# Kernel tuning notes

Measured on AMD Instinct MI355X. Metric: run time of the kernel, lower is better.

## Reference

```python
import jax, jax.numpy as jnp
import numpy as np

N_NODES = 10000
N_EDGES = 640000
D_IN = 128
D_OUT = 128


def setup_inputs() -> dict:
    key = jax.random.key(0)
    k1, k2, k3, k4 = jax.random.split(key, 4)
    x = jax.random.normal(k1, (N_NODES, D_IN), dtype=jnp.float32)
    # PyG GCNConv weight: [dim_out, dim_in] (glorot)
    W = jax.random.normal(k2, (D_OUT, D_IN), dtype=jnp.float32) * (1.0 / np.sqrt(D_IN))
    b = jnp.zeros((D_OUT,), dtype=jnp.float32)
    edge_weight = jax.random.uniform(k3, (N_EDGES,), dtype=jnp.float32)
    edge_index = jax.random.randint(k4, (2, N_EDGES), 0, N_NODES, dtype=jnp.int32)
    return {"x": x, "W": W, "b": b, "edge_weight": edge_weight, "edge_index": edge_index}


def reference(x, W, b, edge_weight, edge_index):
    N = x.shape[0]
    # --- add self loops (fill weight = 1.0), PyG default ---
    loops = jnp.arange(N, dtype=edge_index.dtype)
    src = jnp.concatenate([edge_index[0], loops])
    dst = jnp.concatenate([edge_index[1], loops])
    ew = jnp.concatenate([edge_weight, jnp.ones((N,), dtype=edge_weight.dtype)])
    # --- symmetric GCN normalization: deg from target index ---
    deg = jax.ops.segment_sum(ew, dst, num_segments=N)
    dinv = jnp.where(deg > 0, jax.lax.rsqrt(deg), 0.0)
    norm = dinv[src] * ew * dinv[dst]  # [E+N]
    # --- linear transform then gather-scale-scatter aggregation ---
    h = x @ W.T  # [N, D_OUT]
    msgs = h[src] * norm[:, None]  # [E+N, D_OUT]
    out = jax.ops.segment_sum(msgs, dst, num_segments=N)
    return out + b
```

## Files before the change

### kernel.cpp

```cpp
#include <hip/hip_runtime.h>

#define N_NODES 10000
#define N_EDGES 640000
#define D 128
#define CAP 128

typedef unsigned long long ull;
typedef unsigned short u16;
typedef unsigned int u32;

#define CHUNKS 256
#define EPC 2500
#define GEMM_NPB 32
#define GEMM_BLOCKS ((N_NODES + GEMM_NPB - 1) / GEMM_NPB)
#define SMEM_BYTES 40000
#define EW_FX 131072.0f
#define CNT_SH 24
#define EW_MASK 0xffffffu
#define EWQ_FX 262144.0f
#define SRC_MASK 0x3fffu

__device__ __forceinline__ u16 f2bf(float f) {
    unsigned u = __float_as_uint(f);
    unsigned r = (u + 0x7fffu + ((u >> 16) & 1u)) >> 16;
    return (u16)r;
}


__global__ void __launch_bounds__(256) k_hist_fill_gemm(
    const int* __restrict__ src, const int* __restrict__ dst,
    const float* __restrict__ ew, u32* __restrict__ gcw,
    const float* __restrict__ x, const float* __restrict__ W,
    u16* __restrict__ h_bf, u32* __restrict__ csr)
{
    extern __shared__ char smem[];
    const int t = threadIdx.x;

    if (blockIdx.x < CHUNKS) {
        u32* hist = (u32*)smem;
        for (int i = t; i < N_NODES; i += 256) hist[i] = 0;
        __syncthreads();

        const int e0 = blockIdx.x * EPC;
        u32 dlr[10];
        #pragma unroll
        for (int i = 0; i < 10; ++i) {
            int idx = i * 256 + t;
            dlr[i] = 0xffffffffu;
            if (idx < EPC) {
                int e = e0 + idx;
                int d = dst[e];
                u32 add = (1u << CNT_SH) | (u32)(ew[e] * EW_FX + 0.5f);
                u32 old = atomicAdd(&hist[d], add);
                dlr[i] = ((u32)d << 7) | ((old >> CNT_SH) & 127u);
            }
        }
        __syncthreads();

        for (int i = t; i < N_NODES; i += 256) {
            u32 v = hist[i];
            if (v) {
                u32 old = atomicAdd(&gcw[i], v);
                hist[i] = old >> CNT_SH;
            }
        }
        __syncthreads();

        #pragma unroll
        for (int i = 0; i < 10; ++i) {
            if (dlr[i] != 0xffffffffu) {
                int e = e0 + i * 256 + t;
                int d = (int)(dlr[i] >> 7);
                int lr = (int)(dlr[i] & 127u);
                int slot = (int)hist[d] + lr;
                u32 ewq = (u32)(ew[e] * EWQ_FX);
                csr[(size_t)d * CAP + slot] = (ewq << 14) | (u32)src[e];
            }
        }
    } else {
        float* xs = (float*)smem;
        const int gb = blockIdx.x - CHUNKS;
        const int node0 = gb * GEMM_NPB;
        const int col = t & 127;
        const int half = t >> 7;

        #pragma unroll
        for (int r = 0; r < 16; ++r) {
            int row = half * 16 + r;
            int n = node0 + row;
            xs[row * D + col] = (n < N_NODES) ? x[n * D + col] : 0.0f;
        }
        __syncthreads();

        float acc[16];
        #pragma unroll
        for (int r = 0; r < 16; ++r) acc[r] = 0.0f;

        const float4* Wrow = (const float4*)&W[col * D];
        const float* xbase = &xs[half * 16 * D];
        for (int k4 = 0; k4 < D / 4; ++k4) {
            float4 w = Wrow[k4];
            int k = k4 * 4;
            #pragma unroll
            for (int r = 0; r < 16; ++r) {
                acc[r] += xbase[r * D + k + 0] * w.x;
                acc[r] += xbase[r * D + k + 1] * w.y;
                acc[r] += xbase[r * D + k + 2] * w.z;
                acc[r] += xbase[r * D + k + 3] * w.w;
            }
        }
        #pragma unroll
        for (int r = 0; r < 16; ++r) {
            int n = node0 + half * 16 + r;
            if (n < N_NODES) h_bf[n * D + col] = f2bf(acc[r]);
        }
    }
}


__global__ void __launch_bounds__(256) k_agg(
    const u32* __restrict__ gcw, const u32* __restrict__ csr,
    const u16* __restrict__ h_bf, const float* __restrict__ bias,
    float* __restrict__ out)
{
    const int n = blockIdx.x * 4 + (threadIdx.x >> 6);
    const int lane = threadIdx.x & 63;
    const int slice = lane >> 4;
    const int li = lane & 15;

    const u32 gn = gcw[n];
    const int deg = (int)(gn >> CNT_SH);
    const float dn = rsqrtf(1.0f + (float)(gn & EW_MASK) * (1.0f / EW_FX));
    const u32* bucket = csr + (size_t)n * CAP;

    float acc[8];
    #pragma unroll
    for (int k = 0; k < 8; ++k) acc[k] = 0.0f;

    for (int j = slice; j < deg; j += 4) {
        u32 v = bucket[j];
        int s = (int)(v & SRC_MASK);
        float w = (float)(v >> 14) * (1.0f / EWQ_FX);
        u32 gs = gcw[s];
        float ds_ = rsqrtf(1.0f + (float)(gs & EW_MASK) * (1.0f / EW_FX));
        float nm = ds_ * w * dn;
        union { float4 f4; unsigned u[4]; } uu;
        uu.f4 = *(const float4*)(h_bf + (size_t)s * D + li * 8);
        #pragma unroll
        for (int k = 0; k < 4; ++k) {
            acc[2 * k]     += __uint_as_float(uu.u[k] << 16) * nm;
            acc[2 * k + 1] += __uint_as_float(uu.u[k] & 0xffff0000u) * nm;
        }
    }
    #pragma unroll
    for (int k = 0; k < 8; ++k) {
        acc[k] += __shfl_xor(acc[k], 16);
        acc[k] += __shfl_xor(acc[k], 32);
    }
    if (slice == 0) {
        float s2 = dn * dn;
        union { float4 f4; unsigned u[4]; } hh;
        hh.f4 = *(const float4*)(h_bf + (size_t)n * D + li * 8);
        const float4* b4 = (const float4*)(bias + li * 8);
        float4 b0 = b4[0], b1 = b4[1];
        float4 o0, o1;
        o0.x = acc[0] + __uint_as_float(hh.u[0] << 16) * s2 + b0.x;
        o0.y = acc[1] + __uint_as_float(hh.u[0] & 0xffff0000u) * s2 + b0.y;
        o0.z = acc[2] + __uint_as_float(hh.u[1] << 16) * s2 + b0.z;
        o0.w = acc[3] + __uint_as_float(hh.u[1] & 0xffff0000u) * s2 + b0.w;
        o1.x = acc[4] + __uint_as_float(hh.u[2] << 16) * s2 + b1.x;
        o1.y = acc[5] + __uint_as_float(hh.u[2] & 0xffff0000u) * s2 + b1.y;
        o1.z = acc[6] + __uint_as_float(hh.u[3] << 16) * s2 + b1.z;
        o1.w = acc[7] + __uint_as_float(hh.u[3] & 0xffff0000u) * s2 + b1.w;
        float4* o4 = (float4*)(out + (size_t)n * D + li * 8);
        o4[0] = o0;
        o4[1] = o1;
    }
}


extern "C" void kernel_launch(void* const* d_in, const int* in_sizes, int n_in,
                              void* d_out, int out_size, void* d_ws, size_t ws_size,
                              hipStream_t stream) {
    const float* x  = (const float*)d_in[0];
    const float* W  = (const float*)d_in[1];
    const float* b  = (const float*)d_in[2];
    const float* ew = (const float*)d_in[3];
    const int* ei   = (const int*)d_in[4];
    const int* src = ei;
    const int* dst = ei + N_EDGES;
    float* out = (float*)d_out;

    char* ws = (char*)d_ws;
    u32*   gcw  = (u32*)(ws);
    u16*   h_bf = (u16*)(ws + 40000);
    u32*   csr  = (u32*)(ws + 2600000);

    hipMemsetAsync(gcw, 0, 40000, stream);
    k_hist_fill_gemm<<<CHUNKS + GEMM_BLOCKS, 256, SMEM_BYTES, stream>>>(
        src, dst, ew, gcw, x, W, h_bf, csr);
    k_agg<<<N_NODES / 4, 256, 0, stream>>>(gcw, csr, h_bf, b, out);
}
```

Baseline: 124.0 us.

## Replace shared-memory histogram bucketing with direct global atomics per edge

The edge-bucketing path drops the per-block shared-memory histogram (40 KB LDS, three sync phases, per-chunk global flush). Each edge now does one global atomicAdd on its destination counter and writes its CSR slot directly. GEMM blocks are placed first in the grid and LDS drops to 16 KB, which should raise occupancy. The cost is 640K global atomics, contended on average about 64 per node, in place of roughly 10K per chunk.

```diff
diff --git a/kernel.cpp b/kernel.cpp
--- a/kernel.cpp
+++ b/kernel.cpp
@@ -9,11 +9,10 @@
 typedef unsigned short u16;
 typedef unsigned int u32;
 
-#define CHUNKS 256
-#define EPC 2500
 #define GEMM_NPB 32
 #define GEMM_BLOCKS ((N_NODES + GEMM_NPB - 1) / GEMM_NPB)
-#define SMEM_BYTES 40000
+#define EDGE_BLOCKS 1250
+#define SMEM_BYTES 16384
 #define EW_FX 131072.0f
 #define CNT_SH 24
 #define EW_MASK 0xffffffu
@@ -27,7 +26,7 @@
 }
 
 
-__global__ void __launch_bounds__(256) k_hist_fill_gemm(
+__global__ void __launch_bounds__(256) k_main(
     const int* __restrict__ src, const int* __restrict__ dst,
     const float* __restrict__ ew, u32* __restrict__ gcw,
     const float* __restrict__ x, const float* __restrict__ W,
@@ -36,51 +35,9 @@
     extern __shared__ char smem[];
     const int t = threadIdx.x;
 
-    if (blockIdx.x < CHUNKS) {
-        u32* hist = (u32*)smem;
-        for (int i = t; i < N_NODES; i += 256) hist[i] = 0;
-        __syncthreads();
-
-        const int e0 = blockIdx.x * EPC;
-        u32 dlr[10];
-        #pragma unroll
-        for (int i = 0; i < 10; ++i) {
-            int idx = i * 256 + t;
-            dlr[i] = 0xffffffffu;
-            if (idx < EPC) {
-                int e = e0 + idx;
-                int d = dst[e];
-                u32 add = (1u << CNT_SH) | (u32)(ew[e] * EW_FX + 0.5f);
-                u32 old = atomicAdd(&hist[d], add);
-                dlr[i] = ((u32)d << 7) | ((old >> CNT_SH) & 127u);
-            }
-        }
-        __syncthreads();
-
-        for (int i = t; i < N_NODES; i += 256) {
-            u32 v = hist[i];
-            if (v) {
-                u32 old = atomicAdd(&gcw[i], v);
-                hist[i] = old >> CNT_SH;
-            }
-        }
-        __syncthreads();
-
-        #pragma unroll
-        for (int i = 0; i < 10; ++i) {
-            if (dlr[i] != 0xffffffffu) {
-                int e = e0 + i * 256 + t;
-                int d = (int)(dlr[i] >> 7);
-                int lr = (int)(dlr[i] & 127u);
-                int slot = (int)hist[d] + lr;
-                u32 ewq = (u32)(ew[e] * EWQ_FX);
-                csr[(size_t)d * CAP + slot] = (ewq << 14) | (u32)src[e];
-            }
-        }
-    } else {
+    if (blockIdx.x < GEMM_BLOCKS) {
         float* xs = (float*)smem;
-        const int gb = blockIdx.x - CHUNKS;
-        const int node0 = gb * GEMM_NPB;
+        const int node0 = blockIdx.x * GEMM_NPB;
         const int col = t & 127;
         const int half = t >> 7;
 
@@ -113,6 +70,19 @@
         for (int r = 0; r < 16; ++r) {
             int n = node0 + half * 16 + r;
             if (n < N_NODES) h_bf[n * D + col] = f2bf(acc[r]);
+        }
+    } else {
+        const int base = (blockIdx.x - GEMM_BLOCKS) * 512;
+        #pragma unroll
+        for (int i = 0; i < 2; ++i) {
+            int e = base + i * 256 + t;
+            int d = dst[e];
+            float w = ew[e];
+            u32 add = (1u << CNT_SH) | (u32)(w * EW_FX + 0.5f);
+            u32 old = atomicAdd(&gcw[d], add);
+            int slot = (int)(old >> CNT_SH);
+            u32 ewq = (u32)(w * EWQ_FX);
+            csr[(size_t)d * CAP + slot] = (ewq << 14) | (u32)src[e];
         }
     }
 }
@@ -197,7 +167,7 @@
     u32*   csr  = (u32*)(ws + 2600000);
 
     hipMemsetAsync(gcw, 0, 40000, stream);
-    k_hist_fill_gemm<<<CHUNKS + GEMM_BLOCKS, 256, SMEM_BYTES, stream>>>(
+    k_main<<<GEMM_BLOCKS + EDGE_BLOCKS, 256, SMEM_BYTES, stream>>>(
         src, dst, ew, gcw, x, W, h_bf, csr);
     k_agg<<<N_NODES / 4, 256, 0, stream>>>(gcw, csr, h_bf, b, out);
 }
```

After: 145.6 us. +17.5%, slower.
